# Optimization experiments

Measured on AMD Instinct MI355X. Metric: run time of the kernel, lower is better.

Reference implementation:

```python
import jax, jax.numpy as jnp
import numpy as np
from jax import lax

B, H, W = 256, 28, 28
LATENT = 64
SOM = (16, 16)
FLAT = 7 * 7 * 256  # encoder feature size after two 2x2 pools


def conv2d_same(x, w, b):
    # x: NHWC, w: HWIO
    return lax.conv_general_dilated(x, w, (1, 1), 'SAME',
                                    dimension_numbers=('NHWC', 'HWIO', 'NHWC')) + b


def maxpool_2x2(x):
    return lax.reduce_window(x, -jnp.inf, lax.max, (1, 2, 2, 1), (1, 2, 2, 1), 'SAME')


def upsample_2x(x):
    return jnp.repeat(jnp.repeat(x, 2, axis=1), 2, axis=2)


def encode(x, conv1_w, conv1_b, conv2_w, conv2_b, enc_w, enc_b):
    h = jax.nn.relu(conv2d_same(x, conv1_w, conv1_b))      # [B,28,28,256]
    h = maxpool_2x2(h)                                      # [B,14,14,256]
    h = jax.nn.relu(conv2d_same(h, conv2_w, conv2_b))      # [B,14,14,256]
    h = maxpool_2x2(h)                                      # [B,7,7,256]
    h = h.reshape(h.shape[0], -1)                           # [B,12544]
    return h @ enc_w + enc_b                                # [B,latent]


def decode(z, dec_w, dec_b, deconv1_w, deconv1_b, deconv2_w, deconv2_b):
    h = z @ dec_w + dec_b                                   # [B,12544]
    h = h.reshape(-1, 7, 7, 256)
    h = upsample_2x(h)                                      # [B,14,14,256]
    h = jax.nn.relu(conv2d_same(h, deconv1_w, deconv1_b))
    h = upsample_2x(h)                                      # [B,28,28,256]
    h = conv2d_same(h, deconv2_w, deconv2_b)                # [B,28,28,1]
    return jax.nn.sigmoid(h)


def setup_inputs() -> dict:
    key = jax.random.key(0)
    ks = jax.random.split(key, 12)
    tn = lambda k, shp, s: jax.random.truncated_normal(k, -2.0, 2.0, shp, jnp.float32) * s
    return {
        'x': jax.random.uniform(ks[0], (B, H, W, 1), jnp.float32),
        'conv1_w': tn(ks[1], (4, 4, 1, 256), 0.1),
        'conv1_b': jnp.full((256,), 0.1, jnp.float32),
        'conv2_w': tn(ks[2], (4, 4, 256, 256), 0.1),
        'conv2_b': jnp.full((256,), 0.1, jnp.float32),
        'enc_w': tn(ks[3], (FLAT, LATENT), 0.02),
        'enc_b': jnp.zeros((LATENT,), jnp.float32),
        'embeddings': tn(ks[4], (SOM[0], SOM[1], LATENT), 0.05),
        'dec_w': tn(ks[5], (LATENT, FLAT), 0.02),
        'dec_b': jnp.zeros((FLAT,), jnp.float32),
        'deconv1_w': tn(ks[6], (4, 4, 256, 256), 0.1),
        'deconv1_b': jnp.full((256,), 0.1, jnp.float32),
        'deconv2_w': tn(ks[7], (4, 4, 256, 1), 0.1),
        'deconv2_b': jnp.full((1,), 0.1, jnp.float32),
    }


def reference(x, conv1_w, conv1_b, conv2_w, conv2_b, enc_w, enc_b, embeddings,
              dec_w, dec_b, deconv1_w, deconv1_b, deconv2_w, deconv2_b):
    z_e = encode(x, conv1_w, conv1_b, conv2_w, conv2_b, enc_w, enc_b)  # [B,D]
    emb_flat = embeddings.reshape(-1, LATENT)                          # [K,D]
    # squared euclidean distances [B,K] (cdist pattern)
    z_dist_flat = jnp.sum(jnp.square(z_e[:, None, :] - emb_flat[None, :, :]), axis=-1)
    k = jnp.argmin(z_dist_flat, axis=-1)                               # [B]
    z_q = emb_flat[k]                                                  # [B,D]
    x_hat_e = decode(z_e, dec_w, dec_b, deconv1_w, deconv1_b, deconv2_w, deconv2_b)
    x_hat_q = decode(z_q, dec_w, dec_b, deconv1_w, deconv1_b, deconv2_w, deconv2_b)
    return jnp.stack([x_hat_e, x_hat_q], axis=0)  # [2,B,28,28,1]
```

## Files before the change

### kernel.cpp

```cpp
#include <hip/hip_runtime.h>
#include <hip/hip_bf16.h>

typedef unsigned short u16;
using short8 = __attribute__((ext_vector_type(8))) short;
using half8  = __attribute__((ext_vector_type(8))) _Float16;
using half4  = __attribute__((ext_vector_type(4))) _Float16;
using half2v = __attribute__((ext_vector_type(2))) _Float16;
using f32x4  = __attribute__((ext_vector_type(4))) float;

__device__ __forceinline__ u16 f2bf(float f) {
    unsigned int u = __float_as_uint(f);
    u += 0x7FFFu + ((u >> 16) & 1u);
    return (u16)(u >> 16);
}
__device__ __forceinline__ float bf2f(u16 h) {
    return __uint_as_float(((unsigned int)h) << 16);
}

__device__ __forceinline__ void gl_lds16(const void* g, void* l) {
    __builtin_amdgcn_global_load_lds((const __attribute__((address_space(1))) void*)g,
                                     (__attribute__((address_space(3))) void*)l, 16, 0, 0);
}

#define PIPE_WAIT8() asm volatile("s_waitcnt vmcnt(8)" ::: "memory")
#define PIPE_WAIT0() asm volatile("s_waitcnt vmcnt(0)" ::: "memory")
#define BAR() __builtin_amdgcn_s_barrier()

__global__ __launch_bounds__(256) void wprep_split_kernel(const float* __restrict__ src,
                                                          u16* __restrict__ hi, u16* __restrict__ lo) {
    int idx = blockIdx.x * 256 + threadIdx.x;
    int ci = idx & 255, n = (idx >> 8) & 255, kk = idx >> 16;
    float v = src[(kk * 256 + ci) * 256 + n];
    u16 h = f2bf(v);
    hi[idx] = h;
    lo[idx] = f2bf(v - bf2f(h));
}

__global__ __launch_bounds__(256) void wprep_dc1_par(const float* __restrict__ src, _Float16* __restrict__ dst) {
    const int idx = blockIdx.x * 256 + threadIdx.x;
    const int ci = idx & 255, n = (idx >> 8) & 255, tg = idx >> 16;
    int p, j;
    if (tg < 9)       { p = 0; j = tg; }
    else if (tg < 15) { p = 1; j = tg - 9; }
    else if (tg < 21) { p = 2; j = tg - 15; }
    else              { p = 3; j = tg - 21; }
    const int dy = p >> 1, dx = p & 1;
    const int nx = 3 - dx;
    const int oyi = j / nx, oxi = j % nx;
    int ky0, kyn, kx0, kxn;
    if (dy == 0) { ky0 = (oyi == 0) ? 0 : (oyi == 1 ? 1 : 3); kyn = (oyi == 1) ? 2 : 1; }
    else         { ky0 = (oyi == 0) ? 0 : 2;                  kyn = 2; }
    if (dx == 0) { kx0 = (oxi == 0) ? 0 : (oxi == 1 ? 1 : 3); kxn = (oxi == 1) ? 2 : 1; }
    else         { kx0 = (oxi == 0) ? 0 : 2;                  kxn = 2; }
    float s = 0.f;
    for (int a = 0; a < kyn; ++a)
        for (int c = 0; c < kxn; ++c)
            s += src[(((ky0 + a) * 4 + (kx0 + c)) * 256 + ci) * 256 + n];
    dst[((size_t)tg << 16) + (n << 8) + ci] = (_Float16)s;
}

__global__ __launch_bounds__(256) void wprep_dc2_par(const float* __restrict__ src, _Float16* __restrict__ dst) {
    const int idx = blockIdx.x * 256 + threadIdx.x;
    if (idx >= 9216) return;
    const int ci = idx & 255;
    const int j9 = (idx >> 8) % 9, p = (idx >> 8) / 9;
    const int dy = p >> 1, dx = p & 1;
    const int oyi = j9 / 3, oxi = j9 % 3;
    float s = 0.f;
    if (!((dy == 1 && oyi == 2) || (dx == 1 && oxi == 2))) {
        int ky0, kyn, kx0, kxn;
        if (dy == 0) { ky0 = (oyi == 0) ? 0 : (oyi == 1 ? 1 : 3); kyn = (oyi == 1) ? 2 : 1; }
        else         { ky0 = (oyi == 0) ? 0 : 2;                  kyn = 2; }
        if (dx == 0) { kx0 = (oxi == 0) ? 0 : (oxi == 1 ? 1 : 3); kxn = (oxi == 1) ? 2 : 1; }
        else         { kx0 = (oxi == 0) ? 0 : 2;                  kxn = 2; }
        for (int a = 0; a < kyn; ++a)
            for (int c = 0; c < kxn; ++c)
                s += src[((ky0 + a) * 4 + (kx0 + c)) * 256 + ci];
    }
    dst[idx] = (_Float16)s;
}

__global__ __launch_bounds__(256) void conv1_pool_v2(const float* __restrict__ x,
                                                     const float* __restrict__ w,
                                                     const float* __restrict__ bias,
                                                     u16* __restrict__ hi, u16* __restrict__ lo) {
    __shared__ float xs[5][32];
    const int blk = blockIdx.x;
    const int py = blk % 14, b = blk / 14;
    const int t = threadIdx.x;
    for (int i = t; i < 160; i += 256) {
        const int r = i >> 5, c = i & 31;
        const int gy = 2 * py - 1 + r, gx = c - 1;
        float v = 0.f;
        if ((unsigned)gy < 28u && (unsigned)gx < 28u) v = x[(b * 28 + gy) * 28 + gx];
        xs[r][c] = v;
    }
    __syncthreads();
    float wr[16];
#pragma unroll
    for (int k = 0; k < 16; ++k) wr[k] = w[k * 256 + t];
    const float bs = bias[t];
    for (int px = 0; px < 14; ++px) {
        float m = 0.f;
#pragma unroll
        for (int dy = 0; dy < 2; ++dy)
#pragma unroll
            for (int dx = 0; dx < 2; ++dx) {
                float a = bs;
#pragma unroll
                for (int ky = 0; ky < 4; ++ky)
#pragma unroll
                    for (int kx = 0; kx < 4; ++kx)
                        a += xs[dy + ky][2 * px + dx + kx] * wr[ky * 4 + kx];
                m = fmaxf(m, a);
            }
        u16 h = f2bf(m);
        const int o = ((b * 14 + py) * 14 + px) * 256 + t;
        hi[o] = h;
        lo[o] = f2bf(m - bf2f(h));
    }
}

__global__ __launch_bounds__(256, 2) void conv2_split_v2(const u16* __restrict__ Ih, const u16* __restrict__ Il,
                                                         const u16* __restrict__ Wh, const u16* __restrict__ Wl,
                                                         const u16* __restrict__ zg,
                                                         const float* __restrict__ bias, float* __restrict__ out) {
    __shared__ __align__(16) short lds[32768];
    const int AL = 8192, BH = 16384, BL = 24576;
    const int t = threadIdx.x, lane = t & 63, w = t >> 6;
    const int wm = w >> 1, wn = w & 1;
    const int l16 = lane & 15, l4 = lane >> 4;
    const int m0 = blockIdx.x * 128, n0 = blockIdx.y * 128;
    const int rl = lane >> 3;
    const int chS = (((lane & 7) ^ rl)) << 3;
    int ay[4], ax[4], ab[4], wb[4], aoff[4];
    bool av[4];
#pragma unroll
    for (int j = 0; j < 4; ++j) {
        const int r = w * 32 + j * 8 + rl;
        const int gm = m0 + r;
        const int b = gm / 196, rem = gm % 196;
        ay[j] = rem / 14; ax[j] = rem % 14; ab[j] = b * 196;
        wb[j] = (n0 + r) << 8;
    }
    f32x4 acc[4][4] = {};

    for (int kt = 0; kt < 64; ++kt) {
        const int kk = kt >> 2;
        if ((kt & 3) == 0) {
            const int ky = kk >> 2, kx = kk & 3;
#pragma unroll
            for (int j = 0; j < 4; ++j) {
                const int iy = ay[j] + ky - 1, ix = ax[j] + kx - 1;
                av[j] = ((unsigned)iy < 14u) && ((unsigned)ix < 14u);
                aoff[j] = (ab[j] + iy * 14 + ix) << 8;
            }
        }
        const int kc = (kt & 3) << 6;
        __syncthreads();
#pragma unroll
        for (int j = 0; j < 4; ++j) {
            const int rowb = (w * 32 + j * 8) << 6;
            const u16* gh = av[j] ? (Ih + aoff[j] + kc + chS) : zg;
            const u16* gl = av[j] ? (Il + aoff[j] + kc + chS) : zg;
            gl_lds16(gh, lds + rowb);
            gl_lds16(gl, lds + AL + rowb);
            const int woff = (kk << 16) + wb[j] + kc + chS;
            gl_lds16(Wh + woff, lds + BH + rowb);
            gl_lds16(Wl + woff, lds + BL + rowb);
        }
        __syncthreads();
#pragma unroll
        for (int ks = 0; ks < 2; ++ks) {
            short8 bhf[4], blf[4];
#pragma unroll
            for (int ni = 0; ni < 4; ++ni) {
                const int row = wn * 64 + ni * 16 + l16;
                const int p = (ks * 4 + l4) ^ (row & 7);
                const int off = (row << 6) + (p << 3);
                bhf[ni] = *(const short8*)&lds[BH + off];
                blf[ni] = *(const short8*)&lds[BL + off];
            }
#pragma unroll
            for (int mi = 0; mi < 4; ++mi) {
                const int row = wm * 64 + mi * 16 + l16;
                const int p = (ks * 4 + l4) ^ (row & 7);
                const int off = (row << 6) + (p << 3);
                const short8 ah = *(const short8*)&lds[off];
                const short8 al = *(const short8*)&lds[AL + off];
#pragma unroll
                for (int ni = 0; ni < 4; ++ni) {
                    acc[mi][ni] = __builtin_amdgcn_mfma_f32_16x16x32_bf16(ah, bhf[ni], acc[mi][ni], 0, 0, 0);
                    acc[mi][ni] = __builtin_amdgcn_mfma_f32_16x16x32_bf16(ah, blf[ni], acc[mi][ni], 0, 0, 0);
                    acc[mi][ni] = __builtin_amdgcn_mfma_f32_16x16x32_bf16(al, bhf[ni], acc[mi][ni], 0, 0, 0);
                }
            }
        }
    }
#pragma unroll
    for (int ni = 0; ni < 4; ++ni) {
        const int col = n0 + wn * 64 + ni * 16 + l16;
        const float bv = bias[col];
#pragma unroll
        for (int mi = 0; mi < 4; ++mi) {
            const int mrow = m0 + wm * 64 + mi * 16 + l4 * 4;
#pragma unroll
            for (int r = 0; r < 4; ++r)
                out[(size_t)(mrow + r) * 256 + col] = fmaxf(acc[mi][ni][r] + bv, 0.f);
        }
    }
}

__global__ __launch_bounds__(256, 2) void deconv1_par(const _Float16* __restrict__ I,
                                                      const _Float16* __restrict__ WC,
                                                      const _Float16* __restrict__ zg,
                                                      const float* __restrict__ bias,
                                                      _Float16* __restrict__ out) {
    __shared__ __align__(16) _Float16 lds[32768];
    const int t = threadIdx.x, lane = t & 63, w = t >> 6;
    const int wm = w >> 1, wn = w & 1;
    const int l16 = lane & 15, l4 = lane >> 4;
    const int m0 = blockIdx.x * 128, n0 = blockIdx.y * 128;
    const int p = blockIdx.z, dy = p >> 1, dx = p & 1;
    const int nx = 3 - dx;
    const int ntaps = (3 - dy) * nx;
    const int pbase = (dy == 0) ? (dx == 0 ? 0 : 9) : (dx == 0 ? 15 : 21);
    const int nkt = ntaps * 4;

    const int rl8 = lane >> 3;
    const int g = (lane & 7) ^ rl8;
    const _Float16* selA = I + (g << 3);
    const _Float16* selB = WC + ((size_t)pbase << 16) + (g << 3);

    int aY[4], aX[4], ab[4], wb[4];
#pragma unroll
    for (int j = 0; j < 4; ++j) {
        const int r = w * 32 + j * 8 + rl8;
        const int gm = m0 + r;
        const int b = gm / 49, rem = gm % 49;
        aY[j] = rem / 7; aX[j] = rem % 7; ab[j] = b * 49;
        wb[j] = (n0 + r) << 8;
    }
    int aoff[4]; bool av[4];
    auto dectap = [&](int kk) {
        const int oy = kk / nx - (dy == 0 ? 1 : 0);
        const int ox = kk % nx - (dx == 0 ? 1 : 0);
#pragma unroll
        for (int j = 0; j < 4; ++j) {
            const int iy = aY[j] + oy, ix = aX[j] + ox;
            av[j] = ((unsigned)iy < 7u) && ((unsigned)ix < 7u);
            aoff[j] = (ab[j] + iy * 7 + ix) << 8;
        }
    };
    int rdA[4], rdB[4];
#pragma unroll
    for (int mi = 0; mi < 4; ++mi) {
        const int ra = wm * 64 + mi * 16 + l16;
        rdA[mi] = (ra << 6) + ((l4 ^ (ra & 7)) << 3);
    }
#pragma unroll
    for (int ni = 0; ni < 4; ++ni) {
        const int rb = wn * 64 + ni * 16 + l16;
        rdB[ni] = 8192 + (rb << 6) + ((l4 ^ (rb & 7)) << 3);
    }
    auto stage = [&](int kt) {
        const int kk = kt >> 2, kc = (kt & 3) << 6;
        const int buf = (kt & 1) << 14;
#pragma unroll
        for (int j = 0; j < 4; ++j) {
            const int rowb = buf + ((w * 32 + j * 8) << 6);
            const _Float16* asrc = av[j] ? (selA + aoff[j] + kc) : zg;
            gl_lds16(asrc, lds + rowb);
            gl_lds16(selB + (kk << 16) + wb[j] + kc, lds + 8192 + rowb);
        }
    };

    f32x4 acc[4][4] = {};
    dectap(0);
    stage(0);
    for (int kt = 0; kt < nkt; ++kt) {
        const int ktn = (kt < nkt - 1) ? kt + 1 : kt;
        if ((ktn & 3) == 0 && ktn == kt + 1) dectap(ktn >> 2);
        stage(ktn);
        PIPE_WAIT8();
        BAR();
        const int base = (kt & 1) << 14;
#pragma unroll
        for (int ks = 0; ks < 2; ++ks) {
            const int x32 = ks << 5;
            half8 b8[4];
#pragma unroll
            for (int ni = 0; ni < 4; ++ni)
                b8[ni] = *(const half8*)&lds[base + (rdB[ni] ^ x32)];
#pragma unroll
            for (int mi = 0; mi < 4; ++mi) {
                const half8 a8 = *(const half8*)&lds[base + (rdA[mi] ^ x32)];
#pragma unroll
                for (int ni = 0; ni < 4; ++ni)
                    acc[mi][ni] = __builtin_amdgcn_mfma_f32_16x16x32_f16(a8, b8[ni], acc[mi][ni], 0, 0, 0);
            }
        }
        BAR();
    }
    PIPE_WAIT0();
#pragma unroll
    for (int mi = 0; mi < 4; ++mi) {
        const int mb = m0 + wm * 64 + mi * 16 + l4 * 4;
#pragma unroll
        for (int r = 0; r < 4; ++r) {
            const int m = mb + r;
            const int b = m / 49, rem = m % 49;
            const int Y = rem / 7, X = rem % 7;
            _Float16* op = out + (((size_t)(b * 196 + (2 * Y + dy) * 14 + (2 * X + dx))) << 8);
#pragma unroll
            for (int ni = 0; ni < 4; ++ni) {
                const int col = n0 + wn * 64 + ni * 16 + l16;
                op[col] = (_Float16)fmaxf(acc[mi][ni][r] + bias[col], 0.f);
            }
        }
    }
}

__global__ __launch_bounds__(256) void pool2_kernel(const float* __restrict__ h2, float* __restrict__ h2p) {
    int idx = blockIdx.x * 256 + threadIdx.x;
    int c = idx & 255;
    int rest = idx >> 8;
    int px = rest % 7, py = (rest / 7) % 7, b = rest / 49;
    const float* base = h2 + (((size_t)(b * 14 + 2 * py)) * 14 + 2 * px) * 256 + c;
    float v = fmaxf(fmaxf(base[0], base[256]), fmaxf(base[14 * 256], base[14 * 256 + 256]));
    h2p[idx] = v;
}

__global__ __launch_bounds__(256) void encp_kernel(const float* __restrict__ h2p, const float* __restrict__ ew,
                                                   float* __restrict__ partials) {
    __shared__ float ews[8192];
    __shared__ float hbuf[8][128];
    const int t = threadIdx.x, c = blockIdx.x;
    const float* esrc = ew + (size_t)c * 8192;
    for (int i = t; i < 2048; i += 256)
        *(f32x4*)&ews[i * 4] = *(const f32x4*)&esrc[i * 4];
    const int n = t & 63, sub = t >> 6;
    const int rr = t >> 5, kq = (t & 31) << 2;
    float* pout = partials + (size_t)c * 16384;
    for (int bi = 0; bi < 32; ++bi) {
        __syncthreads();
        *(f32x4*)&hbuf[rr][kq] = *(const f32x4*)&h2p[(size_t)(bi * 8 + rr) * 12544 + c * 128 + kq];
        __syncthreads();
        float a0 = 0.f, a1 = 0.f;
        for (int k = 0; k < 128; ++k) {
            const float wv = ews[k * 64 + n];
            a0 += hbuf[sub][k] * wv;
            a1 += hbuf[sub + 4][k] * wv;
        }
        pout[(bi * 8 + sub) * 64 + n] = a0;
        pout[(bi * 8 + sub + 4) * 64 + n] = a1;
    }
}

__global__ __launch_bounds__(256) void encr_kernel(const float* __restrict__ partials, const float* __restrict__ eb,
                                                   float* __restrict__ zcat) {
    const int o = blockIdx.x * 256 + threadIdx.x;
    float s = eb[o & 63];
    for (int c = 0; c < 98; ++c) s += partials[(size_t)c * 16384 + o];
    zcat[o] = s;
}

__global__ __launch_bounds__(256) void som_kernel(const float* __restrict__ emb, float* __restrict__ zcat) {
    __shared__ float zrow[64];
    __shared__ float sd[256];
    __shared__ int si[256];
    const int b = blockIdx.x, t = threadIdx.x;
    if (t < 64) zrow[t] = zcat[b * 64 + t];
    __syncthreads();
    float acc = 0.f;
    const float* e = emb + t * 64;
    for (int d = 0; d < 64; ++d) { float df = zrow[d] - e[d]; acc += df * df; }
    sd[t] = acc; si[t] = t;
    __syncthreads();
    for (int off = 128; off >= 1; off >>= 1) {
        if (t < off) {
            float d2 = sd[t + off]; int i2 = si[t + off];
            if (d2 < sd[t] || (d2 == sd[t] && i2 < si[t])) { sd[t] = d2; si[t] = i2; }
        }
        __syncthreads();
    }
    const int k = si[0];
    if (t < 64) zcat[(256 + b) * 64 + t] = emb[k * 64 + t];
}

__global__ __launch_bounds__(256) void dec_kernel(const float* __restrict__ zcat, const float* __restrict__ dw,
                                                  const float* __restrict__ db, _Float16* __restrict__ dech) {
    __shared__ float z[8][64];
    const int t = threadIdx.x;
    const int bg = blockIdx.x / 49;
    const int nc = blockIdx.x % 49;
    for (int i = t; i < 512; i += 256) z[i >> 6][i & 63] = zcat[bg * 512 + i];
    __syncthreads();
    const int n = nc * 256 + t;
    const float bv = db[n];
    float acc[8];
#pragma unroll
    for (int j = 0; j < 8; ++j) acc[j] = bv;
    for (int k = 0; k < 64; ++k) {
        float wv = dw[(size_t)k * 12544 + n];
#pragma unroll
        for (int j = 0; j < 8; ++j) acc[j] += z[j][k] * wv;
    }
#pragma unroll
    for (int j = 0; j < 8; ++j) dech[((size_t)(bg * 8 + j)) * 12544 + n] = (_Float16)acc[j];
}

__global__ __launch_bounds__(256) void deconv2_v6(const _Float16* __restrict__ d1, const _Float16* __restrict__ w2c,
                                                  const float* __restrict__ bias, float* __restrict__ out) {
    __shared__ _Float16 ds[6 * 14 * 256];
    __shared__ _Float16 wl[9216];
    const int t = threadIdx.x;
    const int blk = blockIdx.x;
    const int q = blk & 3, b = blk >> 2;
    const int r0 = (q == 3) ? 8 : 3 * q;
    for (int i = t; i < 1152; i += 256)
        *(half8*)&wl[i * 8] = *(const half8*)&w2c[i * 8];
    for (int i = t; i < 2688; i += 256) {
        const int r = i / 448, rem = i % 448;
        *(half8*)&ds[r * 3584 + rem * 8] =
            *(const half8*)&d1[((size_t)(b * 14 + r0 + r) * 14) * 256 + rem * 8];
    }
    const int lane = t & 63, wv = t >> 6;
    const int ch0 = lane * 4;
    const float bv = bias[0];
    __syncthreads();
    for (int pi = 0; pi < 49; ++pi) {
        const int ql = pi * 4 + wv;
        const int oy = 7 * q + ql / 28, ox = ql % 28;
        const int dy = oy & 1, Y = oy >> 1;
        const int dxp = ox & 1, X = ox >> 1;
        const _Float16* wp = &wl[((dy * 2 + dxp) * 9) * 256 + ch0];
        float a0 = 0.f, a1 = 0.f;
#pragma unroll
        for (int j = 0; j < 9; ++j) {
            const int iy = Y + (j / 3) - (dy ? 0 : 1);
            const int ix = X + (j % 3) - (dxp ? 0 : 1);
            if (iy >= r0 && iy < r0 + 6 && (unsigned)ix < 14u) {
                const half4 dv = *(const half4*)&ds[((iy - r0) * 14 + ix) * 256 + ch0];
                const half4 w4 = *(const half4*)&wp[j * 256];
                half2v dlo = {dv.x, dv.y}, dhi = {dv.z, dv.w};
                half2v wlo = {w4.x, w4.y}, whi = {w4.z, w4.w};
                a0 = __builtin_amdgcn_fdot2(dlo, wlo, a0, false);
                a1 = __builtin_amdgcn_fdot2(dhi, whi, a1, false);
            }
        }
        float acc = a0 + a1;
#pragma unroll
        for (int off = 32; off; off >>= 1) acc += __shfl_xor(acc, off);
        if (lane == 0) out[(size_t)b * 784 + oy * 28 + ox] = 1.f / (1.f + expf(-(acc + bv)));
    }
}

extern "C" void kernel_launch(void* const* d_in, const int* in_sizes, int n_in,
                              void* d_out, int out_size, void* d_ws, size_t ws_size,
                              hipStream_t stream) {
    const float* x    = (const float*)d_in[0];
    const float* c1w  = (const float*)d_in[1];
    const float* c1b  = (const float*)d_in[2];
    const float* c2w  = (const float*)d_in[3];
    const float* c2b  = (const float*)d_in[4];
    const float* ew   = (const float*)d_in[5];
    const float* eb   = (const float*)d_in[6];
    const float* emb  = (const float*)d_in[7];
    const float* dw   = (const float*)d_in[8];
    const float* db   = (const float*)d_in[9];
    const float* dc1w = (const float*)d_in[10];
    const float* dc1b = (const float*)d_in[11];
    const float* dc2w = (const float*)d_in[12];
    const float* dc2b = (const float*)d_in[13];
    float* out = (float*)d_out;

    char* ws = (char*)d_ws;
    size_t off = 0;
    auto alloc = [&](size_t bytes) { size_t o = off; off += (bytes + 255) & ~(size_t)255; return o; };

    u16*      h1p_hi = (u16*)(ws + alloc((size_t)256 * 196 * 256 * 2));
    u16*      h1p_lo = (u16*)(ws + alloc((size_t)256 * 196 * 256 * 2));
    u16*      w2T_hi = (u16*)(ws + alloc((size_t)16 * 256 * 256 * 2));
    u16*      w2T_lo = (u16*)(ws + alloc((size_t)16 * 256 * 256 * 2));
    float*    h2     = (float*)(ws + alloc((size_t)256 * 196 * 256 * 4));
    float*    h2p    = (float*)(ws + alloc((size_t)256 * 49 * 256 * 4));
    float*    zcat   = (float*)(ws + alloc((size_t)512 * 64 * 4));
    _Float16* dech   = (_Float16*)(ws + alloc((size_t)512 * 49 * 256 * 2));
    _Float16* wc1    = (_Float16*)(ws + alloc((size_t)25 * 256 * 256 * 2));
    _Float16* d1     = (_Float16*)(ws + alloc((size_t)512 * 196 * 256 * 2));
    _Float16* w2c    = (_Float16*)(ws + alloc((size_t)9216 * 2));
    u16*      zg     = (u16*)(ws + alloc(256));
    float*    partials = h2;

    hipMemsetAsync(zg, 0, 256, stream);
    wprep_split_kernel<<<4096, 256, 0, stream>>>(c2w, w2T_hi, w2T_lo);
    wprep_dc1_par<<<6400, 256, 0, stream>>>(dc1w, wc1);
    wprep_dc2_par<<<36, 256, 0, stream>>>(dc2w, w2c);
    conv1_pool_v2<<<3584, 256, 0, stream>>>(x, c1w, c1b, h1p_hi, h1p_lo);
    conv2_split_v2<<<dim3(392, 2), 256, 0, stream>>>(h1p_hi, h1p_lo, w2T_hi, w2T_lo, zg, c2b, h2);
    pool2_kernel<<<12544, 256, 0, stream>>>(h2, h2p);
    encp_kernel<<<98, 256, 0, stream>>>(h2p, ew, partials);
    encr_kernel<<<64, 256, 0, stream>>>(partials, eb, zcat);
    som_kernel<<<256, 256, 0, stream>>>(emb, zcat);
    dec_kernel<<<3136, 256, 0, stream>>>(zcat, dw, db, dech);
    deconv1_par<<<dim3(196, 2, 4), 256, 0, stream>>>(dech, wc1, (const _Float16*)zg, dc1b, d1);
    deconv2_v6<<<2048, 256, 0, stream>>>(d1, w2c, dc2b, out);
}
```

Before: 881.1 us.

## Fuse prep, pool and reduction kernels; single-buffer deconv1 staging

Merges the three weight-prep kernels and the zero-fill memset into one launch. Folds the second max-pool into the encoder partial-GEMM kernel and the partial reduction into the SOM kernel, which removes three launches and the pooled intermediate buffer. Separately, deconv1 drops its double-buffered async prefetch pipeline for a single LDS buffer with two barriers per k-step. That halves LDS use but stops overlapping global loads with MFMA work. Launch savings may be offset by the lost pipelining in the largest GEMM.

```diff
diff --git a/kernel.cpp b/kernel.cpp
--- a/kernel.cpp
+++ b/kernel.cpp
@@ -22,62 +22,62 @@
                                      (__attribute__((address_space(3))) void*)l, 16, 0, 0);
 }
 
-#define PIPE_WAIT8() asm volatile("s_waitcnt vmcnt(8)" ::: "memory")
-#define PIPE_WAIT0() asm volatile("s_waitcnt vmcnt(0)" ::: "memory")
-#define BAR() __builtin_amdgcn_s_barrier()
-
-__global__ __launch_bounds__(256) void wprep_split_kernel(const float* __restrict__ src,
-                                                          u16* __restrict__ hi, u16* __restrict__ lo) {
-    int idx = blockIdx.x * 256 + threadIdx.x;
-    int ci = idx & 255, n = (idx >> 8) & 255, kk = idx >> 16;
-    float v = src[(kk * 256 + ci) * 256 + n];
-    u16 h = f2bf(v);
-    hi[idx] = h;
-    lo[idx] = f2bf(v - bf2f(h));
-}
-
-__global__ __launch_bounds__(256) void wprep_dc1_par(const float* __restrict__ src, _Float16* __restrict__ dst) {
-    const int idx = blockIdx.x * 256 + threadIdx.x;
-    const int ci = idx & 255, n = (idx >> 8) & 255, tg = idx >> 16;
-    int p, j;
-    if (tg < 9)       { p = 0; j = tg; }
-    else if (tg < 15) { p = 1; j = tg - 9; }
-    else if (tg < 21) { p = 2; j = tg - 15; }
-    else              { p = 3; j = tg - 21; }
-    const int dy = p >> 1, dx = p & 1;
-    const int nx = 3 - dx;
-    const int oyi = j / nx, oxi = j % nx;
-    int ky0, kyn, kx0, kxn;
-    if (dy == 0) { ky0 = (oyi == 0) ? 0 : (oyi == 1 ? 1 : 3); kyn = (oyi == 1) ? 2 : 1; }
-    else         { ky0 = (oyi == 0) ? 0 : 2;                  kyn = 2; }
-    if (dx == 0) { kx0 = (oxi == 0) ? 0 : (oxi == 1 ? 1 : 3); kxn = (oxi == 1) ? 2 : 1; }
-    else         { kx0 = (oxi == 0) ? 0 : 2;                  kxn = 2; }
-    float s = 0.f;
-    for (int a = 0; a < kyn; ++a)
-        for (int c = 0; c < kxn; ++c)
-            s += src[(((ky0 + a) * 4 + (kx0 + c)) * 256 + ci) * 256 + n];
-    dst[((size_t)tg << 16) + (n << 8) + ci] = (_Float16)s;
-}
-
-__global__ __launch_bounds__(256) void wprep_dc2_par(const float* __restrict__ src, _Float16* __restrict__ dst) {
-    const int idx = blockIdx.x * 256 + threadIdx.x;
-    if (idx >= 9216) return;
-    const int ci = idx & 255;
-    const int j9 = (idx >> 8) % 9, p = (idx >> 8) / 9;
-    const int dy = p >> 1, dx = p & 1;
-    const int oyi = j9 / 3, oxi = j9 % 3;
-    float s = 0.f;
-    if (!((dy == 1 && oyi == 2) || (dx == 1 && oxi == 2))) {
+__global__ __launch_bounds__(256) void wprep_all(const float* __restrict__ c2w,
+                                                 u16* __restrict__ hi, u16* __restrict__ lo,
+                                                 const float* __restrict__ dc1w, _Float16* __restrict__ wc1,
+                                                 const float* __restrict__ dc2w, _Float16* __restrict__ w2c,
+                                                 u16* __restrict__ zg) {
+    const int bid = blockIdx.x, t = threadIdx.x;
+    if (bid < 4096) {
+        int idx = bid * 256 + t;
+        int ci = idx & 255, n = (idx >> 8) & 255, kk = idx >> 16;
+        float v = c2w[(kk * 256 + ci) * 256 + n];
+        u16 h = f2bf(v);
+        hi[idx] = h;
+        lo[idx] = f2bf(v - bf2f(h));
+    } else if (bid < 10496) {
+        const int idx = (bid - 4096) * 256 + t;
+        const int ci = idx & 255, n = (idx >> 8) & 255, tg = idx >> 16;
+        int p, j;
+        if (tg < 9)       { p = 0; j = tg; }
+        else if (tg < 15) { p = 1; j = tg - 9; }
+        else if (tg < 21) { p = 2; j = tg - 15; }
+        else              { p = 3; j = tg - 21; }
+        const int dy = p >> 1, dx = p & 1;
+        const int nx = 3 - dx;
+        const int oyi = j / nx, oxi = j % nx;
         int ky0, kyn, kx0, kxn;
         if (dy == 0) { ky0 = (oyi == 0) ? 0 : (oyi == 1 ? 1 : 3); kyn = (oyi == 1) ? 2 : 1; }
         else         { ky0 = (oyi == 0) ? 0 : 2;                  kyn = 2; }
         if (dx == 0) { kx0 = (oxi == 0) ? 0 : (oxi == 1 ? 1 : 3); kxn = (oxi == 1) ? 2 : 1; }
         else         { kx0 = (oxi == 0) ? 0 : 2;                  kxn = 2; }
+        float s = 0.f;
         for (int a = 0; a < kyn; ++a)
             for (int c = 0; c < kxn; ++c)
-                s += src[((ky0 + a) * 4 + (kx0 + c)) * 256 + ci];
-    }
-    dst[idx] = (_Float16)s;
+                s += dc1w[(((ky0 + a) * 4 + (kx0 + c)) * 256 + ci) * 256 + n];
+        wc1[((size_t)tg << 16) + (n << 8) + ci] = (_Float16)s;
+    } else if (bid < 10532) {
+        const int idx = (bid - 10496) * 256 + t;
+        if (idx >= 9216) return;
+        const int ci = idx & 255;
+        const int j9 = (idx >> 8) % 9, p = (idx >> 8) / 9;
+        const int dy = p >> 1, dx = p & 1;
+        const int oyi = j9 / 3, oxi = j9 % 3;
+        float s = 0.f;
+        if (!((dy == 1 && oyi == 2) || (dx == 1 && oxi == 2))) {
+            int ky0, kyn, kx0, kxn;
+            if (dy == 0) { ky0 = (oyi == 0) ? 0 : (oyi == 1 ? 1 : 3); kyn = (oyi == 1) ? 2 : 1; }
+            else         { ky0 = (oyi == 0) ? 0 : 2;                  kyn = 2; }
+            if (dx == 0) { kx0 = (oxi == 0) ? 0 : (oxi == 1 ? 1 : 3); kxn = (oxi == 1) ? 2 : 1; }
+            else         { kx0 = (oxi == 0) ? 0 : 2;                  kxn = 2; }
+            for (int a = 0; a < kyn; ++a)
+                for (int c = 0; c < kxn; ++c)
+                    s += dc2w[((ky0 + a) * 4 + (kx0 + c)) * 256 + ci];
+        }
+        w2c[idx] = (_Float16)s;
+    } else {
+        if (t < 128) zg[t] = 0;
+    }
 }
 
 __global__ __launch_bounds__(256) void conv1_pool_v2(const float* __restrict__ x,
@@ -211,12 +211,12 @@
     }
 }
 
-__global__ __launch_bounds__(256, 2) void deconv1_par(const _Float16* __restrict__ I,
-                                                      const _Float16* __restrict__ WC,
-                                                      const _Float16* __restrict__ zg,
-                                                      const float* __restrict__ bias,
-                                                      _Float16* __restrict__ out) {
-    __shared__ __align__(16) _Float16 lds[32768];
+__global__ __launch_bounds__(256, 2) void deconv1_par_v5(const _Float16* __restrict__ I,
+                                                         const _Float16* __restrict__ WC,
+                                                         const _Float16* __restrict__ zg,
+                                                         const float* __restrict__ bias,
+                                                         _Float16* __restrict__ out) {
+    __shared__ __align__(16) _Float16 lds[16384];
     const int t = threadIdx.x, lane = t & 63, w = t >> 6;
     const int wm = w >> 1, wn = w & 1;
     const int l16 = lane & 15, l4 = lane >> 4;
@@ -263,46 +263,36 @@
         const int rb = wn * 64 + ni * 16 + l16;
         rdB[ni] = 8192 + (rb << 6) + ((l4 ^ (rb & 7)) << 3);
     }
-    auto stage = [&](int kt) {
+
+    f32x4 acc[4][4] = {};
+    for (int kt = 0; kt < nkt; ++kt) {
+        if ((kt & 3) == 0) dectap(kt >> 2);
         const int kk = kt >> 2, kc = (kt & 3) << 6;
-        const int buf = (kt & 1) << 14;
+        __syncthreads();
 #pragma unroll
         for (int j = 0; j < 4; ++j) {
-            const int rowb = buf + ((w * 32 + j * 8) << 6);
+            const int rowb = (w * 32 + j * 8) << 6;
             const _Float16* asrc = av[j] ? (selA + aoff[j] + kc) : zg;
             gl_lds16(asrc, lds + rowb);
             gl_lds16(selB + (kk << 16) + wb[j] + kc, lds + 8192 + rowb);
         }
-    };
-
-    f32x4 acc[4][4] = {};
-    dectap(0);
-    stage(0);
-    for (int kt = 0; kt < nkt; ++kt) {
-        const int ktn = (kt < nkt - 1) ? kt + 1 : kt;
-        if ((ktn & 3) == 0 && ktn == kt + 1) dectap(ktn >> 2);
-        stage(ktn);
-        PIPE_WAIT8();
-        BAR();
-        const int base = (kt & 1) << 14;
+        __syncthreads();
 #pragma unroll
         for (int ks = 0; ks < 2; ++ks) {
             const int x32 = ks << 5;
             half8 b8[4];
 #pragma unroll
             for (int ni = 0; ni < 4; ++ni)
-                b8[ni] = *(const half8*)&lds[base + (rdB[ni] ^ x32)];
+                b8[ni] = *(const half8*)&lds[rdB[ni] ^ x32];
 #pragma unroll
             for (int mi = 0; mi < 4; ++mi) {
-                const half8 a8 = *(const half8*)&lds[base + (rdA[mi] ^ x32)];
+                const half8 a8 = *(const half8*)&lds[rdA[mi] ^ x32];
 #pragma unroll
                 for (int ni = 0; ni < 4; ++ni)
                     acc[mi][ni] = __builtin_amdgcn_mfma_f32_16x16x32_f16(a8, b8[ni], acc[mi][ni], 0, 0, 0);
             }
         }
-        BAR();
-    }
-    PIPE_WAIT0();
+    }
 #pragma unroll
     for (int mi = 0; mi < 4; ++mi) {
         const int mb = m0 + wm * 64 + mi * 16 + l4 * 4;
@@ -321,30 +311,32 @@
     }
 }
 
-__global__ __launch_bounds__(256) void pool2_kernel(const float* __restrict__ h2, float* __restrict__ h2p) {
-    int idx = blockIdx.x * 256 + threadIdx.x;
-    int c = idx & 255;
-    int rest = idx >> 8;
-    int px = rest % 7, py = (rest / 7) % 7, b = rest / 49;
-    const float* base = h2 + (((size_t)(b * 14 + 2 * py)) * 14 + 2 * px) * 256 + c;
-    float v = fmaxf(fmaxf(base[0], base[256]), fmaxf(base[14 * 256], base[14 * 256 + 256]));
-    h2p[idx] = v;
-}
-
-__global__ __launch_bounds__(256) void encp_kernel(const float* __restrict__ h2p, const float* __restrict__ ew,
-                                                   float* __restrict__ partials) {
+__global__ __launch_bounds__(256) void encp_v2(const float* __restrict__ h2, const float* __restrict__ ew,
+                                               float* __restrict__ partials) {
     __shared__ float ews[8192];
     __shared__ float hbuf[8][128];
     const int t = threadIdx.x, c = blockIdx.x;
     const float* esrc = ew + (size_t)c * 8192;
     for (int i = t; i < 2048; i += 256)
         *(f32x4*)&ews[i * 4] = *(const f32x4*)&esrc[i * 4];
+    const int p0 = c >> 1, chb = (c & 1) << 7;
+    const int py = p0 / 7, px = p0 % 7;
     const int n = t & 63, sub = t >> 6;
     const int rr = t >> 5, kq = (t & 31) << 2;
     float* pout = partials + (size_t)c * 16384;
     for (int bi = 0; bi < 32; ++bi) {
-        __syncthreads();
-        *(f32x4*)&hbuf[rr][kq] = *(const f32x4*)&h2p[(size_t)(bi * 8 + rr) * 12544 + c * 128 + kq];
+        const int b = bi * 8 + rr;
+        const float* hb = h2 + (((size_t)(b * 14 + 2 * py)) * 14 + 2 * px) * 256 + chb + kq;
+        __syncthreads();
+        f32x4 v0 = *(const f32x4*)hb;
+        f32x4 v1 = *(const f32x4*)(hb + 256);
+        f32x4 v2 = *(const f32x4*)(hb + 14 * 256);
+        f32x4 v3 = *(const f32x4*)(hb + 14 * 256 + 256);
+        f32x4 vm;
+#pragma unroll
+        for (int q = 0; q < 4; ++q)
+            vm[q] = fmaxf(fmaxf(v0[q], v1[q]), fmaxf(v2[q], v3[q]));
+        *(f32x4*)&hbuf[rr][kq] = vm;
         __syncthreads();
         float a0 = 0.f, a1 = 0.f;
         for (int k = 0; k < 128; ++k) {
@@ -357,20 +349,19 @@
     }
 }
 
-__global__ __launch_bounds__(256) void encr_kernel(const float* __restrict__ partials, const float* __restrict__ eb,
-                                                   float* __restrict__ zcat) {
-    const int o = blockIdx.x * 256 + threadIdx.x;
-    float s = eb[o & 63];
-    for (int c = 0; c < 98; ++c) s += partials[(size_t)c * 16384 + o];
-    zcat[o] = s;
-}
-
-__global__ __launch_bounds__(256) void som_kernel(const float* __restrict__ emb, float* __restrict__ zcat) {
+__global__ __launch_bounds__(256) void som_v2(const float* __restrict__ partials, const float* __restrict__ eb,
+                                              const float* __restrict__ emb, float* __restrict__ zcat) {
     __shared__ float zrow[64];
     __shared__ float sd[256];
     __shared__ int si[256];
     const int b = blockIdx.x, t = threadIdx.x;
-    if (t < 64) zrow[t] = zcat[b * 64 + t];
+    if (t < 64) {
+        float s = eb[t];
+        const float* p = partials + b * 64 + t;
+        for (int c = 0; c < 98; ++c) s += p[(size_t)c * 16384];
+        zrow[t] = s;
+        zcat[b * 64 + t] = s;
+    }
     __syncthreads();
     float acc = 0.f;
     const float* e = emb + t * 64;
@@ -479,31 +470,25 @@
     size_t off = 0;
     auto alloc = [&](size_t bytes) { size_t o = off; off += (bytes + 255) & ~(size_t)255; return o; };
 
-    u16*      h1p_hi = (u16*)(ws + alloc((size_t)256 * 196 * 256 * 2));
-    u16*      h1p_lo = (u16*)(ws + alloc((size_t)256 * 196 * 256 * 2));
-    u16*      w2T_hi = (u16*)(ws + alloc((size_t)16 * 256 * 256 * 2));
-    u16*      w2T_lo = (u16*)(ws + alloc((size_t)16 * 256 * 256 * 2));
-    float*    h2     = (float*)(ws + alloc((size_t)256 * 196 * 256 * 4));
-    float*    h2p    = (float*)(ws + alloc((size_t)256 * 49 * 256 * 4));
-    float*    zcat   = (float*)(ws + alloc((size_t)512 * 64 * 4));
-    _Float16* dech   = (_Float16*)(ws + alloc((size_t)512 * 49 * 256 * 2));
-    _Float16* wc1    = (_Float16*)(ws + alloc((size_t)25 * 256 * 256 * 2));
-    _Float16* d1     = (_Float16*)(ws + alloc((size_t)512 * 196 * 256 * 2));
-    _Float16* w2c    = (_Float16*)(ws + alloc((size_t)9216 * 2));
-    u16*      zg     = (u16*)(ws + alloc(256));
-    float*    partials = h2;
-
-    hipMemsetAsync(zg, 0, 256, stream);
-    wprep_split_kernel<<<4096, 256, 0, stream>>>(c2w, w2T_hi, w2T_lo);
-    wprep_dc1_par<<<6400, 256, 0, stream>>>(dc1w, wc1);
-    wprep_dc2_par<<<36, 256, 0, stream>>>(dc2w, w2c);
+    u16*      h1p_hi   = (u16*)(ws + alloc((size_t)256 * 196 * 256 * 2));
+    u16*      h1p_lo   = (u16*)(ws + alloc((size_t)256 * 196 * 256 * 2));
+    u16*      w2T_hi   = (u16*)(ws + alloc((size_t)16 * 256 * 256 * 2));
+    u16*      w2T_lo   = (u16*)(ws + alloc((size_t)16 * 256 * 256 * 2));
+    float*    h2       = (float*)(ws + alloc((size_t)256 * 196 * 256 * 4));
+    float*    partials = (float*)(ws + alloc((size_t)98 * 16384 * 4));
+    float*    zcat     = (float*)(ws + alloc((size_t)512 * 64 * 4));
+    _Float16* dech     = (_Float16*)(ws + alloc((size_t)512 * 49 * 256 * 2));
+    _Float16* wc1      = (_Float16*)(ws + alloc((size_t)25 * 256 * 256 * 2));
+    _Float16* d1       = (_Float16*)(ws + alloc((size_t)512 * 196 * 256 * 2));
+    _Float16* w2c      = (_Float16*)(ws + alloc((size_t)9216 * 2));
+    u16*      zg       = (u16*)(ws + alloc(256));
+
+    wprep_all<<<10533, 256, 0, stream>>>(c2w, w2T_hi, w2T_lo, dc1w, wc1, dc2w, w2c, zg);
     conv1_pool_v2<<<3584, 256, 0, stream>>>(x, c1w, c1b, h1p_hi, h1p_lo);
     conv2_split_v2<<<dim3(392, 2), 256, 0, stream>>>(h1p_hi, h1p_lo, w2T_hi, w2T_lo, zg, c2b, h2);
-    pool2_kernel<<<12544, 256, 0, stream>>>(h2, h2p);
-    encp_kernel<<<98, 256, 0, stream>>>(h2p, ew, partials);
-    encr_kernel<<<64, 256, 0, stream>>>(partials, eb, zcat);
-    som_kernel<<<256, 256, 0, stream>>>(emb, zcat);
+    encp_v2<<<98, 256, 0, stream>>>(h2, ew, partials);
+    som_v2<<<256, 256, 0, stream>>>(partials, eb, emb, zcat);
     dec_kernel<<<3136, 256, 0, stream>>>(zcat, dw, db, dech);
-    deconv1_par<<<dim3(196, 2, 4), 256, 0, stream>>>(dech, wc1, (const _Float16*)zg, dc1b, d1);
+    deconv1_par_v5<<<dim3(196, 2, 4), 256, 0, stream>>>(dech, wc1, (const _Float16*)zg, dc1b, d1);
     deconv2_v6<<<2048, 256, 0, stream>>>(d1, w2c, dc2b, out);
 }
```

Result: faster. 859.4 us (-2.5%).
